# Kernel tuning notes

Hardware: AMD Instinct MI355X
Metric: run time of the kernel (lower is better)

## Reference

```python
import jax, jax.numpy as jnp
import numpy as np

RADIUS = 0.25
NUM_NEIGHBORS = 32
POS_DIM = 24
STEM_C = 64
PATCH_C = 256
LN_EPS = 1e-5


def query_ball_point(radius, nsample, xyz, new_xyz):
    # xyz: [B,N,3], new_xyz: [B,S,3] -> idx [B,S,nsample] (PointNet++ ball query)
    N = xyz.shape[1]
    sqr = (jnp.sum(new_xyz ** 2, -1)[:, :, None]
           + jnp.sum(xyz ** 2, -1)[:, None, :]
           - 2.0 * jnp.einsum('bsd,bnd->bsn', new_xyz, xyz))  # [B,S,N]
    idx = jnp.broadcast_to(jnp.arange(N, dtype=jnp.int32), sqr.shape)
    idx = jnp.where(sqr > radius * radius, N, idx)
    idx = jnp.sort(idx, axis=-1)[..., :nsample]  # first nsample in-ball (by index order)
    first = idx[..., :1]
    idx = jnp.where(idx == N, first, idx)  # pad empty slots with first neighbor
    return idx


def index_points(points, idx):
    # points [B,N,C], idx [B,S,K] -> [B,S,K,C]
    return jax.vmap(lambda p, i: p[i])(points, idx)


def rel_pos_encoding(rel_xyz, dim=POS_DIM):
    # sinusoidal Fourier encoding of 3D offsets: 3 coords * 2 (sin,cos) * dim//6 freqs
    nf = dim // 6
    freqs = 2.0 ** jnp.arange(nf, dtype=rel_xyz.dtype)
    ang = rel_xyz[..., None] * freqs  # [...,3,nf]
    enc = jnp.concatenate([jnp.sin(ang), jnp.cos(ang)], axis=-1)  # [...,3,2nf]
    return enc.reshape(rel_xyz.shape[:-1] + (dim,))


def point_mlp(x, W, b, gamma, beta, activate):
    h = jnp.einsum('...i,io->...o', x, W) + b
    mu = jnp.mean(h, -1, keepdims=True)
    var = jnp.mean((h - mu) ** 2, -1, keepdims=True)
    h = (h - mu) * jax.lax.rsqrt(var + LN_EPS) * gamma + beta
    return jax.nn.gelu(h, approximate=False) if activate else h


def setup_inputs() -> dict:
    key = jax.random.key(0)
    ks = jax.random.split(key, 8)
    B, N, S = 8, 16384, 1024
    in_c = STEM_C + 3 + POS_DIM  # 91
    return {
        'xyz': jax.random.uniform(ks[0], (B, N, 3), dtype=jnp.float32),
        'point_feature': jax.random.normal(ks[1], (B, N, STEM_C), dtype=jnp.float32),
        'patch_center': jax.random.uniform(ks[2], (B, S, 3), dtype=jnp.float32),
        'W1': jax.random.normal(ks[3], (in_c, PATCH_C), dtype=jnp.float32) * 0.02,
        'b1': jnp.zeros((PATCH_C,), jnp.float32),
        'g1': jnp.ones((PATCH_C,), jnp.float32),
        'be1': jnp.zeros((PATCH_C,), jnp.float32),
        'W2': jax.random.normal(ks[4], (PATCH_C, PATCH_C), dtype=jnp.float32) * 0.02,
        'b2': jnp.zeros((PATCH_C,), jnp.float32),
        'g2': jnp.ones((PATCH_C,), jnp.float32),
        'be2': jnp.zeros((PATCH_C,), jnp.float32),
    }


def reference(xyz, point_feature, patch_center, W1, b1, g1, be1, W2, b2, g2, be2):
    neighbor_idx = query_ball_point(RADIUS, NUM_NEIGHBORS, xyz, patch_center)  # [B,S,K]
    grouped_xyz = index_points(xyz, neighbor_idx)              # [B,S,K,3]
    grouped_feature = index_points(point_feature, neighbor_idx)  # [B,S,K,C]
    relative_xyz = grouped_xyz - patch_center[:, :, None, :]
    relative_position = rel_pos_encoding(relative_xyz)         # [B,S,K,24]
    grouped_input = jnp.concatenate((grouped_feature, relative_xyz, relative_position), axis=-1)
    h = point_mlp(grouped_input, W1, b1, g1, be1, True)
    h = point_mlp(h, W2, b2, g2, be2, False)
    patch_feature = jnp.max(h, axis=2)                         # max over neighbors -> [B,S,PATCH_C]
    return patch_feature, neighbor_idx
```

## Files before the change

### kernel.cpp

```cpp
#include <hip/hip_runtime.h>
#include <math.h>

#define NPTS 16384
#define NPTS_PAD 16896
#define KN 32
#define C 256
#define NQ 8192
#define PF_ELEMS (NQ * C)

#define W1P_ELEMS (3 * 16 * 64 * 8)
#define W2P_ELEMS (8 * 16 * 64 * 8)
#define WP_ELEMS  (W1P_ELEMS + W2P_ELEMS)
#define XYZW_ELEMS (8 * NPTS_PAD)
#define HSTR 264

typedef _Float16 half8 __attribute__((ext_vector_type(8)));
typedef _Float16 half4v __attribute__((ext_vector_type(4)));
typedef _Float16 half2t __attribute__((ext_vector_type(2)));
typedef float f32x4 __attribute__((ext_vector_type(4)));

__device__ __forceinline__ float gelu_tanh(float x) {
    const float t  = x * x;
    const float p2 = fmaf(t, 0.0713548162726f, 1.59576912161f);
    const float e  = __expf(x * p2);
    return x - x * __builtin_amdgcn_rcpf(e + 1.0f);
}

__global__ void prep_kernel(const float* __restrict__ W1,
                            const float* __restrict__ b1,
                            const float* __restrict__ W2,
                            const float* __restrict__ xyz,
                            _Float16* __restrict__ wp,
                            float4* __restrict__ xyzw) {
    const int idx = blockIdx.x * 256 + threadIdx.x;
    if (idx < 96 * 256) {
        const int k = idx >> 8, n = idx & 255;
        const float v = (k < 91) ? W1[k * 256 + n] : ((k == 91) ? b1[n] : 0.0f);
        const int kt = k >> 5, quad = (k >> 3) & 3, j = k & 7;
        const int nt = n >> 4, l15 = n & 15;
        wp[(((kt * 16 + nt) * 64) + quad * 16 + l15) * 8 + j] = (_Float16)v;
    } else if (idx < WP_ELEMS) {
        const int e = idx - 96 * 256;
        const int k = e >> 8, n = e & 255;
        const int kt = k >> 5, quad = (k >> 3) & 3, j = k & 7;
        const int nt = n >> 4, l15 = n & 15;
        wp[W1P_ELEMS + (((kt * 16 + nt) * 64) + quad * 16 + l15) * 8 + j] =
            (_Float16)W2[k * 256 + n];
    } else {
        const int e  = idx - WP_ELEMS;
        const int bb = e / NPTS_PAD;
        const int off = e - bb * NPTS_PAD;
        float4 v;
        if (off < NPTS) {
            const float px = xyz[((size_t)bb * NPTS + off) * 3 + 0];
            const float py = xyz[((size_t)bb * NPTS + off) * 3 + 1];
            const float pz = xyz[((size_t)bb * NPTS + off) * 3 + 2];
            const float sp = __fadd_rn(__fadd_rn(__fmul_rn(px, px), __fmul_rn(py, py)),
                                       __fmul_rn(pz, pz));
            v = make_float4(px, py, pz, sp);
        } else {
            v = make_float4(1e9f, 1e9f, 1e9f, 3e18f);
        }
        xyzw[(size_t)bb * NPTS_PAD + off] = v;
    }
}

__global__ void __launch_bounds__(256, 8)
encoder_fused(const float4* __restrict__ xyzw,
              const float* __restrict__ pf,
              const float* __restrict__ ctr,
              const float* __restrict__ g1, const float* __restrict__ be1,
              const float* __restrict__ b2, const float* __restrict__ g2,
              const float* __restrict__ be2,
              const _Float16* __restrict__ w1p,
              const _Float16* __restrict__ w2p,
              float* __restrict__ out0,
              float* __restrict__ out1) {
    const int q = blockIdx.x;
    const int b = q >> 10;
    const int t = threadIdx.x;
    const int w = t >> 6;
    const int lane = t & 63;
    const int quad = lane >> 4;
    const int l15  = lane & 15;

    __shared__ __align__(16) unsigned char H16raw[KN * HSTR * 2];
    __shared__ __align__(16) _Float16 lnph[4 * 256];
    __shared__ __align__(16) float2 sred[2][16][4];
    __shared__ int nbr[KN];
    __shared__ int wcnt[2][2][4];

    _Float16 (*H16)[HSTR] = (_Float16(*)[HSTR])H16raw;
    _Float16 (*Xs)[104]   = (_Float16(*)[104])H16raw;
    _Float16* g1h  = lnph;
    _Float16* be1h = lnph + 256;
    _Float16* g2h  = lnph + 512;
    _Float16* be2h = lnph + 768;

    lnph[t]       = (_Float16)g1[t];
    lnph[256 + t] = (_Float16)be1[t];
    lnph[512 + t] = (_Float16)g2[t];
    lnph[768 + t] = (_Float16)be2[t];

    const float4* xwb = xyzw + (size_t)b * NPTS_PAD;
    const float cx = ctr[q * 3 + 0];
    const float cy = ctr[q * 3 + 1];
    const float cz = ctr[q * 3 + 2];
    const float sc = __fadd_rn(__fadd_rn(__fmul_rn(cx, cx), __fmul_rn(cy, cy)),
                               __fmul_rn(cz, cz));

    float4 pw0 = xwb[t];
    float4 pw1 = xwb[256 + t];
    int found = 0;
    int par = 0;
    for (int base = 0; base < NPTS; base += 512) {
        const float4 nx0 = xwb[base + 512 + t];
        const float4 nx1 = xwb[base + 768 + t];

        const float dt0 = __fadd_rn(__fadd_rn(__fmul_rn(cx, pw0.x), __fmul_rn(cy, pw0.y)),
                                    __fmul_rn(cz, pw0.z));
        const float sq0 = __fsub_rn(__fadd_rn(sc, pw0.w), __fmul_rn(2.0f, dt0));
        const float dt1 = __fadd_rn(__fadd_rn(__fmul_rn(cx, pw1.x), __fmul_rn(cy, pw1.y)),
                                    __fmul_rn(cz, pw1.z));
        const float sq1 = __fsub_rn(__fadd_rn(sc, pw1.w), __fmul_rn(2.0f, dt1));
        const bool in0 = (sq0 <= 0.0625f);
        const bool in1 = (sq1 <= 0.0625f);

        const unsigned long long m0 = __ballot(in0);
        const unsigned long long m1 = __ballot(in1);
        if (lane == 0) {
            wcnt[par][0][w] = (int)__popcll(m0);
            wcnt[par][1][w] = (int)__popcll(m1);
        }
        __syncthreads();
        const int c00 = wcnt[par][0][0], c01 = wcnt[par][0][1];
        const int c02 = wcnt[par][0][2], c03 = wcnt[par][0][3];
        const int c10 = wcnt[par][1][0], c11 = wcnt[par][1][1];
        const int c12 = wcnt[par][1][2], c13 = wcnt[par][1][3];
        int pre0 = found;
        if (w > 0) pre0 += c00;
        if (w > 1) pre0 += c01;
        if (w > 2) pre0 += c02;
        const int C0 = c00 + c01 + c02 + c03;
        int pre1 = found + C0;
        if (w > 0) pre1 += c10;
        if (w > 1) pre1 += c11;
        if (w > 2) pre1 += c12;
        const int tot = C0 + c10 + c11 + c12 + c13;
        const unsigned long long lmask = (1ull << lane) - 1ull;
        const int pos0 = pre0 + (int)__popcll(m0 & lmask);
        const int pos1 = pre1 + (int)__popcll(m1 & lmask);
        if (in0 && pos0 < KN) nbr[pos0] = base + t;
        if (in1 && pos1 < KN) nbr[pos1] = base + 256 + t;
        found += tot;
        par ^= 1;
        if (found >= KN) break;
        pw0 = nx0;
        pw1 = nx1;
    }
    __syncthreads();
    const int count = (found < KN) ? found : KN;
    const int first = (count > 0) ? nbr[0] : NPTS;

    if (t < KN)
        out1[(size_t)q * KN + t] = (float)((t < count) ? nbr[t] : first);

    {
        const int k  = t >> 3;
        const int tc = t & 7;
        const int nidx = (k < count) ? nbr[k] : first;
        const int n = (nidx < NPTS) ? nidx : NPTS - 1;
        const float4 pw = xwb[n];
        const float rx = pw.x - cx;
        const float ry = pw.y - cy;
        const float rz = pw.z - cz;
        const float* pfr = pf + ((size_t)b * NPTS + n) * 64;

        const float4 f0 = *(const float4*)(pfr + tc * 8);
        const float4 f1 = *(const float4*)(pfr + tc * 8 + 4);
        half8 hv;
        hv[0] = (_Float16)f0.x; hv[1] = (_Float16)f0.y;
        hv[2] = (_Float16)f0.z; hv[3] = (_Float16)f0.w;
        hv[4] = (_Float16)f1.x; hv[5] = (_Float16)f1.y;
        hv[6] = (_Float16)f1.z; hv[7] = (_Float16)f1.w;
        *(half8*)&Xs[k][tc * 8] = hv;

        half4v ov;
        #pragma unroll
        for (int j = 0; j < 4; ++j) {
            const int cm = tc * 4 + j;
            const int jj = cm - 3;
            const int d  = jj >> 3;
            const int mm = jj & 7;
            const float rsel = (d == 0) ? rx : ((d == 1) ? ry : rz);
            const float f2 = __int_as_float(0x3E22F983 + ((mm & 3) << 23));
            const float arg = fmaf(rsel, f2, (mm >= 4) ? 0.25f : 0.0f);
#if __has_builtin(__builtin_amdgcn_sinf)
            const float sv = __builtin_amdgcn_sinf(arg);
#else
            const float sv = __sinf(arg * 6.2831853071795864f);
#endif
            float v = (cm < 3) ? ((cm == 0) ? rx : ((cm == 1) ? ry : rz)) : sv;
            v = (cm == 27) ? 1.0f : ((cm > 27) ? 0.0f : v);
            ov[j] = (_Float16)v;
        }
        *(half4v*)&Xs[k][64 + tc * 4] = ov;
    }
    __syncthreads();

    f32x4 acc[2][4];

    const int wu = __builtin_amdgcn_readfirstlane(w);
    const _Float16* __restrict__ w1w = w1p + (size_t)(wu * 4) * 512;
    const _Float16* __restrict__ w2w = w2p + (size_t)(wu * 4) * 512;
    const int lo8 = lane * 8;

    #pragma unroll
    for (int mt = 0; mt < 2; ++mt)
        #pragma unroll
        for (int nt = 0; nt < 4; ++nt)
            acc[mt][nt] = (f32x4){0.f, 0.f, 0.f, 0.f};

    #pragma unroll
    for (int kt = 0; kt < 3; ++kt) {
        const half8 x0 = *(const half8*)&Xs[l15][kt * 32 + quad * 8];
        const half8 x1 = *(const half8*)&Xs[16 + l15][kt * 32 + quad * 8];
        #pragma unroll
        for (int nt = 0; nt < 4; ++nt) {
            const half8 wf = *(const half8*)(w1w + (kt * 16 + nt) * 512 + lo8);
            acc[0][nt] = __builtin_amdgcn_mfma_f32_16x16x32_f16(wf, x0, acc[0][nt], 0, 0, 0);
            acc[1][nt] = __builtin_amdgcn_mfma_f32_16x16x32_f16(wf, x1, acc[1][nt], 0, 0, 0);
        }
    }

    float mu0, mu1, rs0, rs1;
    {
        #pragma unroll
        for (int mt = 0; mt < 2; ++mt) {
            float s = 0.0f, s2 = 0.0f;
            #pragma unroll
            for (int nt = 0; nt < 4; ++nt)
                #pragma unroll
                for (int r = 0; r < 4; ++r) {
                    const float v = acc[mt][nt][r];
                    s += v;
                    s2 = fmaf(v, v, s2);
                }
            s  += __shfl_xor(s, 16, 64);  s  += __shfl_xor(s, 32, 64);
            s2 += __shfl_xor(s2, 16, 64); s2 += __shfl_xor(s2, 32, 64);
            if (quad == 0) sred[mt][l15][w] = make_float2(s, s2);
        }
    }
    __syncthreads();
    {
        #pragma unroll
        for (int mt = 0; mt < 2; ++mt) {
            const float4 pA = *(const float4*)&sred[mt][l15][0];
            const float4 pB = *(const float4*)&sred[mt][l15][2];
            const float S = pA.x + pA.z + pB.x + pB.z;
            const float Q = pA.y + pA.w + pB.y + pB.w;
            const float mu = S * (1.0f / 256.0f);
            const float var = fmaf(Q, 1.0f / 256.0f, -mu * mu);
            const float rs = __builtin_amdgcn_rsqf(var + 1e-5f);
            if (mt == 0) { mu0 = mu; rs0 = rs; } else { mu1 = mu; rs1 = rs; }
        }
    }

    #pragma unroll
    for (int nt = 0; nt < 4; ++nt) {
        const int chb = (w * 4 + nt) * 16 + quad * 4;
        const half4v g4h  = *(const half4v*)&g1h[chb];
        const half4v be4h = *(const half4v*)&be1h[chb];
        #pragma unroll
        for (int mt = 0; mt < 2; ++mt) {
            const float mu = (mt == 0) ? mu0 : mu1;
            const float rs = (mt == 0) ? rs0 : rs1;
            half4v h;
            #pragma unroll
            for (int r = 0; r < 4; ++r) {
                const float A = (float)g4h[r] * rs;
                const float y = fmaf(acc[mt][nt][r] - mu, A, (float)be4h[r]);
                h[r] = (_Float16)gelu_tanh(y);
            }
            *(half4v*)&H16[mt * 16 + l15][chb] = h;
        }
    }
    __syncthreads();

    #pragma unroll
    for (int mt = 0; mt < 2; ++mt)
        #pragma unroll
        for (int nt = 0; nt < 4; ++nt)
            acc[mt][nt] = (f32x4){0.f, 0.f, 0.f, 0.f};

    #pragma unroll
    for (int kt = 0; kt < 8; ++kt) {
        const half8 h0 = *(const half8*)&H16[l15][kt * 32 + quad * 8];
        const half8 h1 = *(const half8*)&H16[16 + l15][kt * 32 + quad * 8];
        #pragma unroll
        for (int nt = 0; nt < 4; ++nt) {
            const half8 wf = *(const half8*)(w2w + (kt * 16 + nt) * 512 + lo8);
            acc[0][nt] = __builtin_amdgcn_mfma_f32_16x16x32_f16(wf, h0, acc[0][nt], 0, 0, 0);
            acc[1][nt] = __builtin_amdgcn_mfma_f32_16x16x32_f16(wf, h1, acc[1][nt], 0, 0, 0);
        }
    }

    #pragma unroll
    for (int nt = 0; nt < 4; ++nt) {
        const f32x4 bv = *(const f32x4*)&b2[(w * 4 + nt) * 16 + quad * 4];
        #pragma unroll
        for (int mt = 0; mt < 2; ++mt)
            #pragma unroll
            for (int r = 0; r < 4; ++r)
                acc[mt][nt][r] += bv[r];
    }
    {
        #pragma unroll
        for (int mt = 0; mt < 2; ++mt) {
            float s = 0.0f, s2 = 0.0f;
            #pragma unroll
            for (int nt = 0; nt < 4; ++nt)
                #pragma unroll
                for (int r = 0; r < 4; ++r) {
                    const float v = acc[mt][nt][r];
                    s += v;
                    s2 = fmaf(v, v, s2);
                }
            s  += __shfl_xor(s, 16, 64);  s  += __shfl_xor(s, 32, 64);
            s2 += __shfl_xor(s2, 16, 64); s2 += __shfl_xor(s2, 32, 64);
            if (quad == 0) sred[mt][l15][w] = make_float2(s, s2);
        }
    }
    __syncthreads();
    {
        #pragma unroll
        for (int mt = 0; mt < 2; ++mt) {
            const float4 pA = *(const float4*)&sred[mt][l15][0];
            const float4 pB = *(const float4*)&sred[mt][l15][2];
            const float S = pA.x + pA.z + pB.x + pB.z;
            const float Q = pA.y + pA.w + pB.y + pB.w;
            const float mu = S * (1.0f / 256.0f);
            const float var = fmaf(Q, 1.0f / 256.0f, -mu * mu);
            const float rs = __builtin_amdgcn_rsqf(var + 1e-5f);
            if (mt == 0) { mu0 = mu; rs0 = rs; } else { mu1 = mu; rs1 = rs; }
        }
    }

    #pragma unroll
    for (int nt = 0; nt < 4; ++nt) {
        const int chb = (w * 4 + nt) * 16 + quad * 4;
        const half4v g4h  = *(const half4v*)&g2h[chb];
        const half4v be4h = *(const half4v*)&be2h[chb];
        #pragma unroll
        for (int mt = 0; mt < 2; ++mt) {
            const float mu = (mt == 0) ? mu0 : mu1;
            const float rs = (mt == 0) ? rs0 : rs1;
            half4v h;
            #pragma unroll
            for (int r = 0; r < 4; ++r) {
                const float A = (float)g4h[r] * rs;
                h[r] = (_Float16)fmaf(acc[mt][nt][r] - mu, A, (float)be4h[r]);
            }
            *(half4v*)&H16[mt * 16 + l15][chb] = h;
        }
    }
    __syncthreads();

    if (t < 128) {
        const _Float16* Hf = &H16[0][0];
        half2t mx = *(const half2t*)(Hf + 2 * t);
        #pragma unroll
        for (int r = 1; r < KN; ++r) {
            const half2t v = *(const half2t*)(Hf + r * HSTR + 2 * t);
            mx = __builtin_elementwise_max(mx, v);
        }
        float2 o2;
        o2.x = (float)mx[0];
        o2.y = (float)mx[1];
        *(float2*)&out0[(size_t)q * C + 2 * t] = o2;
    }
}

extern "C" void kernel_launch(void* const* d_in, const int* in_sizes, int n_in,
                              void* d_out, int out_size, void* d_ws, size_t ws_size,
                              hipStream_t stream) {
    const float* xyz = (const float*)d_in[0];
    const float* pf  = (const float*)d_in[1];
    const float* ctr = (const float*)d_in[2];
    const float* W1  = (const float*)d_in[3];
    const float* b1  = (const float*)d_in[4];
    const float* g1  = (const float*)d_in[5];
    const float* be1 = (const float*)d_in[6];
    const float* W2  = (const float*)d_in[7];
    const float* b2  = (const float*)d_in[8];
    const float* g2  = (const float*)d_in[9];
    const float* be2 = (const float*)d_in[10];

    float* out = (float*)d_out;
    _Float16* wp = (_Float16*)d_ws;
    float4* xyzw = (float4*)(wp + WP_ELEMS);

    prep_kernel<<<(WP_ELEMS + XYZW_ELEMS) / 256, 256, 0, stream>>>(W1, b1, W2, xyz, wp, xyzw);
    encoder_fused<<<NQ, 256, 0, stream>>>(xyzw, pf, ctr,
                                          g1, be1, b2, g2, be2,
                                          wp, wp + W1P_ELEMS,
                                          out, out + PF_ELEMS);
}
```

Before: 186.7 us.

## Process two query centers per block to share point scans and weight loads

Each block now handles two adjacent patch centers instead of one. The ball-query scan over the point cloud loads each xyzw chunk once and tests it against both centers, and each MFMA weight fragment is reused for both queries' activations. The grid is halved and launch bounds lowered to 4 blocks/SM to fit the doubled accumulators and shared memory. The cost is higher register pressure and lower occupancy, and the scan continues until both queries have found their neighbors, so a block can run longer than either query alone would need.

```diff
diff --git a/kernel.cpp b/kernel.cpp
--- a/kernel.cpp
+++ b/kernel.cpp
@@ -65,7 +65,7 @@
     }
 }
 
-__global__ void __launch_bounds__(256, 8)
+__global__ void __launch_bounds__(256, 4)
 encoder_fused(const float4* __restrict__ xyzw,
               const float* __restrict__ pf,
               const float* __restrict__ ctr,
@@ -76,22 +76,24 @@
               const _Float16* __restrict__ w2p,
               float* __restrict__ out0,
               float* __restrict__ out1) {
-    const int q = blockIdx.x;
-    const int b = q >> 10;
+    const int q0 = blockIdx.x * 2;
+    const int b = q0 >> 10;
     const int t = threadIdx.x;
     const int w = t >> 6;
     const int lane = t & 63;
     const int quad = lane >> 4;
     const int l15  = lane & 15;
 
-    __shared__ __align__(16) unsigned char H16raw[KN * HSTR * 2];
+    __shared__ __align__(16) unsigned char H16raw[2][KN * HSTR * 2];
     __shared__ __align__(16) _Float16 lnph[4 * 256];
-    __shared__ __align__(16) float2 sred[2][16][4];
-    __shared__ int nbr[KN];
-    __shared__ int wcnt[2][2][4];
-
-    _Float16 (*H16)[HSTR] = (_Float16(*)[HSTR])H16raw;
-    _Float16 (*Xs)[104]   = (_Float16(*)[104])H16raw;
+    __shared__ __align__(16) float2 sred[2][2][16][4];
+    __shared__ int nbr[2][KN];
+    __shared__ int wcnt[2][2][2][4];
+
+    _Float16 (*H16a)[HSTR] = (_Float16(*)[HSTR])H16raw[0];
+    _Float16 (*H16b)[HSTR] = (_Float16(*)[HSTR])H16raw[1];
+    _Float16 (*Xs0)[104]   = (_Float16(*)[104])H16raw[0];
+    _Float16 (*Xs1)[104]   = (_Float16(*)[104])H16raw[1];
     _Float16* g1h  = lnph;
     _Float16* be1h = lnph + 256;
     _Float16* g2h  = lnph + 512;
@@ -103,77 +105,123 @@
     lnph[768 + t] = (_Float16)be2[t];
 
     const float4* xwb = xyzw + (size_t)b * NPTS_PAD;
-    const float cx = ctr[q * 3 + 0];
-    const float cy = ctr[q * 3 + 1];
-    const float cz = ctr[q * 3 + 2];
-    const float sc = __fadd_rn(__fadd_rn(__fmul_rn(cx, cx), __fmul_rn(cy, cy)),
-                               __fmul_rn(cz, cz));
+    const float cxA = ctr[q0 * 3 + 0], cyA = ctr[q0 * 3 + 1], czA = ctr[q0 * 3 + 2];
+    const float cxB = ctr[q0 * 3 + 3], cyB = ctr[q0 * 3 + 4], czB = ctr[q0 * 3 + 5];
+    const float scA = __fadd_rn(__fadd_rn(__fmul_rn(cxA, cxA), __fmul_rn(cyA, cyA)),
+                                __fmul_rn(czA, czA));
+    const float scB = __fadd_rn(__fadd_rn(__fmul_rn(cxB, cxB), __fmul_rn(cyB, cyB)),
+                                __fmul_rn(czB, czB));
 
     float4 pw0 = xwb[t];
     float4 pw1 = xwb[256 + t];
-    int found = 0;
+    int foundA = 0, foundB = 0;
     int par = 0;
     for (int base = 0; base < NPTS; base += 512) {
         const float4 nx0 = xwb[base + 512 + t];
         const float4 nx1 = xwb[base + 768 + t];
 
-        const float dt0 = __fadd_rn(__fadd_rn(__fmul_rn(cx, pw0.x), __fmul_rn(cy, pw0.y)),
-                                    __fmul_rn(cz, pw0.z));
-        const float sq0 = __fsub_rn(__fadd_rn(sc, pw0.w), __fmul_rn(2.0f, dt0));
-        const float dt1 = __fadd_rn(__fadd_rn(__fmul_rn(cx, pw1.x), __fmul_rn(cy, pw1.y)),
-                                    __fmul_rn(cz, pw1.z));
-        const float sq1 = __fsub_rn(__fadd_rn(sc, pw1.w), __fmul_rn(2.0f, dt1));
-        const bool in0 = (sq0 <= 0.0625f);
-        const bool in1 = (sq1 <= 0.0625f);
-
-        const unsigned long long m0 = __ballot(in0);
-        const unsigned long long m1 = __ballot(in1);
+        const float dA0 = __fadd_rn(__fadd_rn(__fmul_rn(cxA, pw0.x), __fmul_rn(cyA, pw0.y)),
+                                    __fmul_rn(czA, pw0.z));
+        const float sA0 = __fsub_rn(__fadd_rn(scA, pw0.w), __fmul_rn(2.0f, dA0));
+        const float dA1 = __fadd_rn(__fadd_rn(__fmul_rn(cxA, pw1.x), __fmul_rn(cyA, pw1.y)),
+                                    __fmul_rn(czA, pw1.z));
+        const float sA1 = __fsub_rn(__fadd_rn(scA, pw1.w), __fmul_rn(2.0f, dA1));
+        const float dB0 = __fadd_rn(__fadd_rn(__fmul_rn(cxB, pw0.x), __fmul_rn(cyB, pw0.y)),
+                                    __fmul_rn(czB, pw0.z));
+        const float sB0 = __fsub_rn(__fadd_rn(scB, pw0.w), __fmul_rn(2.0f, dB0));
+        const float dB1 = __fadd_rn(__fadd_rn(__fmul_rn(cxB, pw1.x), __fmul_rn(cyB, pw1.y)),
+                                    __fmul_rn(czB, pw1.z));
+        const float sB1 = __fsub_rn(__fadd_rn(scB, pw1.w), __fmul_rn(2.0f, dB1));
+        const bool iA0 = (sA0 <= 0.0625f);
+        const bool iA1 = (sA1 <= 0.0625f);
+        const bool iB0 = (sB0 <= 0.0625f);
+        const bool iB1 = (sB1 <= 0.0625f);
+
+        const unsigned long long mA0 = __ballot(iA0);
+        const unsigned long long mA1 = __ballot(iA1);
+        const unsigned long long mB0 = __ballot(iB0);
+        const unsigned long long mB1 = __ballot(iB1);
         if (lane == 0) {
-            wcnt[par][0][w] = (int)__popcll(m0);
-            wcnt[par][1][w] = (int)__popcll(m1);
+            wcnt[par][0][0][w] = (int)__popcll(mA0);
+            wcnt[par][0][1][w] = (int)__popcll(mA1);
+            wcnt[par][1][0][w] = (int)__popcll(mB0);
+            wcnt[par][1][1][w] = (int)__popcll(mB1);
         }
         __syncthreads();
-        const int c00 = wcnt[par][0][0], c01 = wcnt[par][0][1];
-        const int c02 = wcnt[par][0][2], c03 = wcnt[par][0][3];
-        const int c10 = wcnt[par][1][0], c11 = wcnt[par][1][1];
-        const int c12 = wcnt[par][1][2], c13 = wcnt[par][1][3];
-        int pre0 = found;
-        if (w > 0) pre0 += c00;
-        if (w > 1) pre0 += c01;
-        if (w > 2) pre0 += c02;
-        const int C0 = c00 + c01 + c02 + c03;
-        int pre1 = found + C0;
-        if (w > 0) pre1 += c10;
-        if (w > 1) pre1 += c11;
-        if (w > 2) pre1 += c12;
-        const int tot = C0 + c10 + c11 + c12 + c13;
         const unsigned long long lmask = (1ull << lane) - 1ull;
-        const int pos0 = pre0 + (int)__popcll(m0 & lmask);
-        const int pos1 = pre1 + (int)__popcll(m1 & lmask);
-        if (in0 && pos0 < KN) nbr[pos0] = base + t;
-        if (in1 && pos1 < KN) nbr[pos1] = base + 256 + t;
-        found += tot;
+        {
+            const int c00 = wcnt[par][0][0][0], c01 = wcnt[par][0][0][1];
+            const int c02 = wcnt[par][0][0][2], c03 = wcnt[par][0][0][3];
+            const int c10 = wcnt[par][0][1][0], c11 = wcnt[par][0][1][1];
+            const int c12 = wcnt[par][0][1][2], c13 = wcnt[par][0][1][3];
+            int pre0 = foundA;
+            if (w > 0) pre0 += c00;
+            if (w > 1) pre0 += c01;
+            if (w > 2) pre0 += c02;
+            const int C0 = c00 + c01 + c02 + c03;
+            int pre1 = foundA + C0;
+            if (w > 0) pre1 += c10;
+            if (w > 1) pre1 += c11;
+            if (w > 2) pre1 += c12;
+            const int pos0 = pre0 + (int)__popcll(mA0 & lmask);
+            const int pos1 = pre1 + (int)__popcll(mA1 & lmask);
+            if (iA0 && pos0 < KN) nbr[0][pos0] = base + t;
+            if (iA1 && pos1 < KN) nbr[0][pos1] = base + 256 + t;
+            foundA += C0 + c10 + c11 + c12 + c13;
+        }
+        {
+            const int c00 = wcnt[par][1][0][0], c01 = wcnt[par][1][0][1];
+            const int c02 = wcnt[par][1][0][2], c03 = wcnt[par][1][0][3];
+            const int c10 = wcnt[par][1][1][0], c11 = wcnt[par][1][1][1];
+            const int c12 = wcnt[par][1][1][2], c13 = wcnt[par][1][1][3];
+            int pre0 = foundB;
+            if (w > 0) pre0 += c00;
+            if (w > 1) pre0 += c01;
+            if (w > 2) pre0 += c02;
+            const int C0 = c00 + c01 + c02 + c03;
+            int pre1 = foundB + C0;
+            if (w > 0) pre1 += c10;
+            if (w > 1) pre1 += c11;
+            if (w > 2) pre1 += c12;
+            const int pos0 = pre0 + (int)__popcll(mB0 & lmask);
+            const int pos1 = pre1 + (int)__popcll(mB1 & lmask);
+            if (iB0 && pos0 < KN) nbr[1][pos0] = base + t;
+            if (iB1 && pos1 < KN) nbr[1][pos1] = base + 256 + t;
+            foundB += C0 + c10 + c11 + c12 + c13;
+        }
         par ^= 1;
-        if (found >= KN) break;
+        if (foundA >= KN && foundB >= KN) break;
         pw0 = nx0;
         pw1 = nx1;
     }
     __syncthreads();
-    const int count = (found < KN) ? found : KN;
-    const int first = (count > 0) ? nbr[0] : NPTS;
-
-    if (t < KN)
-        out1[(size_t)q * KN + t] = (float)((t < count) ? nbr[t] : first);
-
-    {
+    const int cntA = (foundA < KN) ? foundA : KN;
+    const int cntB = (foundB < KN) ? foundB : KN;
+    const int fstA = (cntA > 0) ? nbr[0][0] : NPTS;
+    const int fstB = (cntB > 0) ? nbr[1][0] : NPTS;
+
+    if (t < 2 * KN) {
+        const int qq = t >> 5, i = t & 31;
+        const int cnt = qq ? cntB : cntA;
+        const int fst = qq ? fstB : fstA;
+        out1[(size_t)(q0 + qq) * KN + i] = (float)((i < cnt) ? nbr[qq][i] : fst);
+    }
+
+    #pragma unroll
+    for (int qq = 0; qq < 2; ++qq) {
         const int k  = t >> 3;
         const int tc = t & 7;
-        const int nidx = (k < count) ? nbr[k] : first;
+        const int cnt = qq ? cntB : cntA;
+        const int fst = qq ? fstB : fstA;
+        const float ccx = qq ? cxB : cxA;
+        const float ccy = qq ? cyB : cyA;
+        const float ccz = qq ? czB : czA;
+        const int nidx = (k < cnt) ? nbr[qq][k] : fst;
         const int n = (nidx < NPTS) ? nidx : NPTS - 1;
         const float4 pw = xwb[n];
-        const float rx = pw.x - cx;
-        const float ry = pw.y - cy;
-        const float rz = pw.z - cz;
+        const float rx = pw.x - ccx;
+        const float ry = pw.y - ccy;
+        const float rz = pw.z - ccz;
         const float* pfr = pf + ((size_t)b * NPTS + n) * 64;
 
         const float4 f0 = *(const float4*)(pfr + tc * 8);
@@ -183,7 +231,8 @@
         hv[2] = (_Float16)f0.z; hv[3] = (_Float16)f0.w;
         hv[4] = (_Float16)f1.x; hv[5] = (_Float16)f1.y;
         hv[6] = (_Float16)f1.z; hv[7] = (_Float16)f1.w;
-        *(half8*)&Xs[k][tc * 8] = hv;
+        if (qq == 0) *(half8*)&Xs0[k][tc * 8] = hv;
+        else         *(half8*)&Xs1[k][tc * 8] = hv;
 
         half4v ov;
         #pragma unroll
@@ -204,11 +253,12 @@
             v = (cm == 27) ? 1.0f : ((cm > 27) ? 0.0f : v);
             ov[j] = (_Float16)v;
         }
-        *(half4v*)&Xs[k][64 + tc * 4] = ov;
-    }
-    __syncthreads();
-
-    f32x4 acc[2][4];
+        if (qq == 0) *(half4v*)&Xs0[k][64 + tc * 4] = ov;
+        else         *(half4v*)&Xs1[k][64 + tc * 4] = ov;
+    }
+    __syncthreads();
+
+    f32x4 acc[2][2][4];
 
     const int wu = __builtin_amdgcn_readfirstlane(w);
     const _Float16* __restrict__ w1w = w1p + (size_t)(wu * 4) * 512;
@@ -216,25 +266,32 @@
     const int lo8 = lane * 8;
 
     #pragma unroll
-    for (int mt = 0; mt < 2; ++mt)
-        #pragma unroll
-        for (int nt = 0; nt < 4; ++nt)
-            acc[mt][nt] = (f32x4){0.f, 0.f, 0.f, 0.f};
+    for (int qq = 0; qq < 2; ++qq)
+        #pragma unroll
+        for (int mt = 0; mt < 2; ++mt)
+            #pragma unroll
+            for (int nt = 0; nt < 4; ++nt)
+                acc[qq][mt][nt] = (f32x4){0.f, 0.f, 0.f, 0.f};
 
     #pragma unroll
     for (int kt = 0; kt < 3; ++kt) {
-        const half8 x0 = *(const half8*)&Xs[l15][kt * 32 + quad * 8];
-        const half8 x1 = *(const half8*)&Xs[16 + l15][kt * 32 + quad * 8];
+        const half8 xA0 = *(const half8*)&Xs0[l15][kt * 32 + quad * 8];
+        const half8 xA1 = *(const half8*)&Xs0[16 + l15][kt * 32 + quad * 8];
+        const half8 xB0 = *(const half8*)&Xs1[l15][kt * 32 + quad * 8];
+        const half8 xB1 = *(const half8*)&Xs1[16 + l15][kt * 32 + quad * 8];
         #pragma unroll
         for (int nt = 0; nt < 4; ++nt) {
             const half8 wf = *(const half8*)(w1w + (kt * 16 + nt) * 512 + lo8);
-            acc[0][nt] = __builtin_amdgcn_mfma_f32_16x16x32_f16(wf, x0, acc[0][nt], 0, 0, 0);
-            acc[1][nt] = __builtin_amdgcn_mfma_f32_16x16x32_f16(wf, x1, acc[1][nt], 0, 0, 0);
-        }
-    }
-
-    float mu0, mu1, rs0, rs1;
-    {
+            acc[0][0][nt] = __builtin_amdgcn_mfma_f32_16x16x32_f16(wf, xA0, acc[0][0][nt], 0, 0, 0);
+            acc[0][1][nt] = __builtin_amdgcn_mfma_f32_16x16x32_f16(wf, xA1, acc[0][1][nt], 0, 0, 0);
+            acc[1][0][nt] = __builtin_amdgcn_mfma_f32_16x16x32_f16(wf, xB0, acc[1][0][nt], 0, 0, 0);
+            acc[1][1][nt] = __builtin_amdgcn_mfma_f32_16x16x32_f16(wf, xB1, acc[1][1][nt], 0, 0, 0);
+        }
+    }
+
+    float mu[2][2], rs[2][2];
+    #pragma unroll
+    for (int qq = 0; qq < 2; ++qq)
         #pragma unroll
         for (int mt = 0; mt < 2; ++mt) {
             float s = 0.0f, s2 = 0.0f;
@@ -242,29 +299,28 @@
             for (int nt = 0; nt < 4; ++nt)
                 #pragma unroll
                 for (int r = 0; r < 4; ++r) {
-                    const float v = acc[mt][nt][r];
+                    const float v = acc[qq][mt][nt][r];
                     s += v;
                     s2 = fmaf(v, v, s2);
                 }
             s  += __shfl_xor(s, 16, 64);  s  += __shfl_xor(s, 32, 64);
             s2 += __shfl_xor(s2, 16, 64); s2 += __shfl_xor(s2, 32, 64);
-            if (quad == 0) sred[mt][l15][w] = make_float2(s, s2);
-        }
-    }
-    __syncthreads();
-    {
+            if (quad == 0) sred[qq][mt][l15][w] = make_float2(s, s2);
+        }
+    __syncthreads();
+    #pragma unroll
+    for (int qq = 0; qq < 2; ++qq)
         #pragma unroll
         for (int mt = 0; mt < 2; ++mt) {
-            const float4 pA = *(const float4*)&sred[mt][l15][0];
-            const float4 pB = *(const float4*)&sred[mt][l15][2];
+            const float4 pA = *(const float4*)&sred[qq][mt][l15][0];
+            const float4 pB = *(const float4*)&sred[qq][mt][l15][2];
             const float S = pA.x + pA.z + pB.x + pB.z;
             const float Q = pA.y + pA.w + pB.y + pB.w;
-            const float mu = S * (1.0f / 256.0f);
-            const float var = fmaf(Q, 1.0f / 256.0f, -mu * mu);
-            const float rs = __builtin_amdgcn_rsqf(var + 1e-5f);
-            if (mt == 0) { mu0 = mu; rs0 = rs; } else { mu1 = mu; rs1 = rs; }
-        }
-    }
+            const float m_ = S * (1.0f / 256.0f);
+            const float var = fmaf(Q, 1.0f / 256.0f, -m_ * m_);
+            mu[qq][mt] = m_;
+            rs[qq][mt] = __builtin_amdgcn_rsqf(var + 1e-5f);
+        }
 
     #pragma unroll
     for (int nt = 0; nt < 4; ++nt) {
@@ -272,36 +328,43 @@
         const half4v g4h  = *(const half4v*)&g1h[chb];
         const half4v be4h = *(const half4v*)&be1h[chb];
         #pragma unroll
-        for (int mt = 0; mt < 2; ++mt) {
-            const float mu = (mt == 0) ? mu0 : mu1;
-            const float rs = (mt == 0) ? rs0 : rs1;
-            half4v h;
-            #pragma unroll
-            for (int r = 0; r < 4; ++r) {
-                const float A = (float)g4h[r] * rs;
-                const float y = fmaf(acc[mt][nt][r] - mu, A, (float)be4h[r]);
-                h[r] = (_Float16)gelu_tanh(y);
+        for (int qq = 0; qq < 2; ++qq)
+            #pragma unroll
+            for (int mt = 0; mt < 2; ++mt) {
+                half4v h;
+                #pragma unroll
+                for (int r = 0; r < 4; ++r) {
+                    const float A = (float)g4h[r] * rs[qq][mt];
+                    const float y = fmaf(acc[qq][mt][nt][r] - mu[qq][mt], A, (float)be4h[r]);
+                    h[r] = (_Float16)gelu_tanh(y);
+                }
+                if (qq == 0) *(half4v*)&H16a[mt * 16 + l15][chb] = h;
+                else         *(half4v*)&H16b[mt * 16 + l15][chb] = h;
             }
-            *(half4v*)&H16[mt * 16 + l15][chb] = h;
-        }
-    }
-    __syncthreads();
-
-    #pragma unroll
-    for (int mt = 0; mt < 2; ++mt)
-        #pragma unroll
-        for (int nt = 0; nt < 4; ++nt)
-            acc[mt][nt] = (f32x4){0.f, 0.f, 0.f, 0.f};
+    }
+    __syncthreads();
+
+    #pragma unroll
+    for (int qq = 0; qq < 2; ++qq)
+        #pragma unroll
+        for (int mt = 0; mt < 2; ++mt)
+            #pragma unroll
+            for (int nt = 0; nt < 4; ++nt)
+                acc[qq][mt][nt] = (f32x4){0.f, 0.f, 0.f, 0.f};
 
     #pragma unroll
     for (int kt = 0; kt < 8; ++kt) {
-        const half8 h0 = *(const half8*)&H16[l15][kt * 32 + quad * 8];
-        const half8 h1 = *(const half8*)&H16[16 + l15][kt * 32 + quad * 8];
+        const half8 hA0 = *(const half8*)&H16a[l15][kt * 32 + quad * 8];
+        const half8 hA1 = *(const half8*)&H16a[16 + l15][kt * 32 + quad * 8];
+        const half8 hB0 = *(const half8*)&H16b[l15][kt * 32 + quad * 8];
+        const half8 hB1 = *(const half8*)&H16b[16 + l15][kt * 32 + quad * 8];
         #pragma unroll
         for (int nt = 0; nt < 4; ++nt) {
             const half8 wf = *(const half8*)(w2w + (kt * 16 + nt) * 512 + lo8);
-            acc[0][nt] = __builtin_amdgcn_mfma_f32_16x16x32_f16(wf, h0, acc[0][nt], 0, 0, 0);
-            acc[1][nt] = __builtin_amdgcn_mfma_f32_16x16x32_f16(wf, h1, acc[1][nt], 0, 0, 0);
+            acc[0][0][nt] = __builtin_amdgcn_mfma_f32_16x16x32_f16(wf, hA0, acc[0][0][nt], 0, 0, 0);
+            acc[0][1][nt] = __builtin_amdgcn_mfma_f32_16x16x32_f16(wf, hA1, acc[0][1][nt], 0, 0, 0);
+            acc[1][0][nt] = __builtin_amdgcn_mfma_f32_16x16x32_f16(wf, hB0, acc[1][0][nt], 0, 0, 0);
+            acc[1][1][nt] = __builtin_amdgcn_mfma_f32_16x16x32_f16(wf, hB1, acc[1][1][nt], 0, 0, 0);
         }
     }
 
@@ -309,12 +372,15 @@
     for (int nt = 0; nt < 4; ++nt) {
         const f32x4 bv = *(const f32x4*)&b2[(w * 4 + nt) * 16 + quad * 4];
         #pragma unroll
-        for (int mt = 0; mt < 2; ++mt)
-            #pragma unroll
-            for (int r = 0; r < 4; ++r)
-                acc[mt][nt][r] += bv[r];
-    }
-    {
+        for (int qq = 0; qq < 2; ++qq)
+            #pragma unroll
+            for (int mt = 0; mt < 2; ++mt)
+                #pragma unroll
+                for (int r = 0; r < 4; ++r)
+                    acc[qq][mt][nt][r] += bv[r];
+    }
+    #pragma unroll
+    for (int qq = 0; qq < 2; ++qq)
         #pragma unroll
         for (int mt = 0; mt < 2; ++mt) {
             float s = 0.0f, s2 = 0.0f;
@@ -322,29 +388,28 @@
             for (int nt = 0; nt < 4; ++nt)
                 #pragma unroll
                 for (int r = 0; r < 4; ++r) {
-                    const float v = acc[mt][nt][r];
+                    const float v = acc[qq][mt][nt][r];
                     s += v;
                     s2 = fmaf(v, v, s2);
                 }
             s  += __shfl_xor(s, 16, 64);  s  += __shfl_xor(s, 32, 64);
             s2 += __shfl_xor(s2, 16, 64); s2 += __shfl_xor(s2, 32, 64);
-            if (quad == 0) sred[mt][l15][w] = make_float2(s, s2);
-        }
-    }
-    __syncthreads();
-    {
+            if (quad == 0) sred[qq][mt][l15][w] = make_float2(s, s2);
+        }
+    __syncthreads();
+    #pragma unroll
+    for (int qq = 0; qq < 2; ++qq)
         #pragma unroll
         for (int mt = 0; mt < 2; ++mt) {
-            const float4 pA = *(const float4*)&sred[mt][l15][0];
-            const float4 pB = *(const float4*)&sred[mt][l15][2];
+            const float4 pA = *(const float4*)&sred[qq][mt][l15][0];
+            const float4 pB = *(const float4*)&sred[qq][mt][l15][2];
             const float S = pA.x + pA.z + pB.x + pB.z;
             const float Q = pA.y + pA.w + pB.y + pB.w;
-            const float mu = S * (1.0f / 256.0f);
-            const float var = fmaf(Q, 1.0f / 256.0f, -mu * mu);
-            const float rs = __builtin_amdgcn_rsqf(var + 1e-5f);
-            if (mt == 0) { mu0 = mu; rs0 = rs; } else { mu1 = mu; rs1 = rs; }
-        }
-    }
+            const float m_ = S * (1.0f / 256.0f);
+            const float var = fmaf(Q, 1.0f / 256.0f, -m_ * m_);
+            mu[qq][mt] = m_;
+            rs[qq][mt] = __builtin_amdgcn_rsqf(var + 1e-5f);
+        }
 
     #pragma unroll
     for (int nt = 0; nt < 4; ++nt) {
@@ -352,32 +417,35 @@
         const half4v g4h  = *(const half4v*)&g2h[chb];
         const half4v be4h = *(const half4v*)&be2h[chb];
         #pragma unroll
-        for (int mt = 0; mt < 2; ++mt) {
-            const float mu = (mt == 0) ? mu0 : mu1;
-            const float rs = (mt == 0) ? rs0 : rs1;
-            half4v h;
-            #pragma unroll
-            for (int r = 0; r < 4; ++r) {
-                const float A = (float)g4h[r] * rs;
-                h[r] = (_Float16)fmaf(acc[mt][nt][r] - mu, A, (float)be4h[r]);
+        for (int qq = 0; qq < 2; ++qq)
+            #pragma unroll
+            for (int mt = 0; mt < 2; ++mt) {
+                half4v h;
+                #pragma unroll
+                for (int r = 0; r < 4; ++r) {
+                    const float A = (float)g4h[r] * rs[qq][mt];
+                    h[r] = (_Float16)fmaf(acc[qq][mt][nt][r] - mu[qq][mt], A, (float)be4h[r]);
+                }
+                if (qq == 0) *(half4v*)&H16a[mt * 16 + l15][chb] = h;
+                else         *(half4v*)&H16b[mt * 16 + l15][chb] = h;
             }
-            *(half4v*)&H16[mt * 16 + l15][chb] = h;
-        }
-    }
-    __syncthreads();
-
-    if (t < 128) {
-        const _Float16* Hf = &H16[0][0];
-        half2t mx = *(const half2t*)(Hf + 2 * t);
+    }
+    __syncthreads();
+
+    {
+        const int qq = t >> 7;
+        const int tt = t & 127;
+        const _Float16* Hf = qq ? &H16b[0][0] : &H16a[0][0];
+        half2t mx = *(const half2t*)(Hf + 2 * tt);
         #pragma unroll
         for (int r = 1; r < KN; ++r) {
-            const half2t v = *(const half2t*)(Hf + r * HSTR + 2 * t);
+            const half2t v = *(const half2t*)(Hf + r * HSTR + 2 * tt);
             mx = __builtin_elementwise_max(mx, v);
         }
         float2 o2;
         o2.x = (float)mx[0];
         o2.y = (float)mx[1];
-        *(float2*)&out0[(size_t)q * C + 2 * t] = o2;
+        *(float2*)&out0[(size_t)(q0 + qq) * C + 2 * tt] = o2;
     }
 }
 
@@ -401,8 +469,8 @@
     float4* xyzw = (float4*)(wp + WP_ELEMS);
 
     prep_kernel<<<(WP_ELEMS + XYZW_ELEMS) / 256, 256, 0, stream>>>(W1, b1, W2, xyz, wp, xyzw);
-    encoder_fused<<<NQ, 256, 0, stream>>>(xyzw, pf, ctr,
-                                          g1, be1, b2, g2, be2,
-                                          wp, wp + W1P_ELEMS,
-                                          out, out + PF_ELEMS);
+    encoder_fused<<<NQ / 2, 256, 0, stream>>>(xyzw, pf, ctr,
+                                              g1, be1, b2, g2, be2,
+                                              wp, wp + W1P_ELEMS,
+                                              out, out + PF_ELEMS);
 }
```

Result: faster. 180.1 us (-3.6%).
